# Kernel optimization log

Measured on AMD Instinct MI355X. Metric: run time of the kernel, lower is better.

## Reference

```python
import jax, jax.numpy as jnp
import numpy as np

DT = 0.1
B_SZ = 8192
T_HIST = 20
LEN_PRED = 30
FEAT = 32
N_LAYERS = 3
# state transition for constant-acceleration model (matches self.F in torch)
F_MAT = np.array([[1.0, DT, DT * DT / 2], [0.0, 1.0, DT], [0.0, 0.0, 1.0]], dtype=np.float32)


def setup_inputs() -> dict:
    key = jax.random.key(0)
    ks = jax.random.split(key, 16)
    # random-walk trajectories as history observations
    hist = jnp.cumsum(jax.random.normal(ks[0], (B_SZ, T_HIST, 2), jnp.float32) * 0.5, axis=1)
    k_lin = 1.0 / np.sqrt(FEAT)
    k_in = 1.0 / np.sqrt(24)

    def u(k, shape, scale):
        return jax.random.uniform(k, shape, jnp.float32, -scale, scale)

    return {
        "hist": hist,
        "max_accel_x": jnp.ones((1,), jnp.float32) * 10.0,
        "max_accel_y": jnp.ones((1,), jnp.float32) * 20.0,
        "velocity_std_x": jnp.ones((1,), jnp.float32) * 10.0,
        "acceleration_std_x": jnp.ones((1,), jnp.float32) * 10.0,
        "R_x_": jnp.array([0.0448], jnp.float32),
        "R_y_": jnp.array([0.001], jnp.float32),
        "G_x": jnp.array([0.0059, 0.2981, 0.0393], jnp.float32),
        "G_y": jnp.array([0.0059, 0.2981, 0.0393], jnp.float32) / 5.0,
        "Win_W": u(ks[1], (FEAT, 24), k_in),
        "Win_b": u(ks[2], (FEAT,), k_in),
        "enc_Wih": u(ks[3], (N_LAYERS, 4 * FEAT, FEAT), k_lin),
        "enc_Whh": u(ks[4], (N_LAYERS, 4 * FEAT, FEAT), k_lin),
        "enc_bih": u(ks[5], (N_LAYERS, 4 * FEAT), k_lin),
        "enc_bhh": u(ks[6], (N_LAYERS, 4 * FEAT), k_lin),
        "dec_Wih": u(ks[7], (N_LAYERS, 4 * FEAT, FEAT), k_lin),
        "dec_Whh": u(ks[8], (N_LAYERS, 4 * FEAT, FEAT), k_lin),
        "dec_bih": u(ks[9], (N_LAYERS, 4 * FEAT), k_lin),
        "dec_bhh": u(ks[10], (N_LAYERS, 4 * FEAT), k_lin),
        "Wout_W": u(ks[11], (4, FEAT), k_lin),
        "Wout_b": u(ks[12], (4,), k_lin),
        "len_pred": LEN_PRED,
    }


def reference(hist, max_accel_x, max_accel_y, velocity_std_x, acceleration_std_x,
              R_x_, R_y_, G_x, G_y, Win_W, Win_b,
              enc_Wih, enc_Whh, enc_bih, enc_bhh,
              dec_Wih, dec_Whh, dec_bih, dec_bhh,
              Wout_W, Wout_b, len_pred):
    B = hist.shape[0]
    F = jnp.asarray(F_MAT)
    R_x = R_x_[0] * R_x_[0]
    R_y = R_y_[0] * R_y_[0]
    Z_x = hist[:, :, 0]
    Z_y = hist[:, :, 1]

    def lstm(x, h, c, Wih, Whh, bih, bhh):
        g = x @ Wih.T + bih + h @ Whh.T + bhh
        i, f, gg, o = jnp.split(g, 4, axis=1)
        c = jax.nn.sigmoid(f) * c + jax.nn.sigmoid(i) * jnp.tanh(gg)
        h = jax.nn.sigmoid(o) * jnp.tanh(c)
        return h, c

    def stack(XP, h, c, Wih, Whh, bih, bhh):
        x = jnp.tanh(XP @ Win_W.T + Win_b)
        hs, cs = [], []
        for j in range(N_LAYERS):
            hj, cj = lstm(x, h[j], c[j], Wih[j], Whh[j], bih[j], bhh[j])
            hs.append(hj)
            cs.append(cj)
            x = cj  # torch code feeds the fresh CELL state to the next layer
        return jnp.stack(hs), jnp.stack(cs)

    def kpred(X, P, Q):
        return X @ F.T, jnp.einsum('ij,bjk,lk->bil', F, P, F) + Q

    def kupdate(X, P, z, R):
        y = z - X[:, 0]                      # innovation (H picks component 0)
        S = P[:, 0, 0] + R                   # innovation covariance (scalar)
        K = P[:, :, 0] / S[:, None]          # Kalman gain (B,3)
        return X + y[:, None] * K, P - K[:, :, None] * P[:, 0:1, :]

    def kinit(z0):
        # torch always calls _kalman_init with is_x=True (default), so both
        # axes use R_x / velocity_std_x / acceleration_std_x
        X = jnp.zeros((B, 3), hist.dtype).at[:, 0].set(z0)
        d = jnp.stack([R_x, velocity_std_x[0] ** 2, acceleration_std_x[0] ** 2])
        P = jnp.zeros((B, 3, 3), hist.dtype).at[:, jnp.arange(3), jnp.arange(3)].set(d)
        return X, P

    Qx_e = jnp.outer(G_x * max_accel_x[0], G_x * max_accel_x[0])
    Qy_e = jnp.outer(G_y * max_accel_y[0], G_y * max_accel_y[0])

    Xx, Px = kinit(Z_x[:, 0])
    Xy, Py = kinit(Z_y[:, 0])
    h = jnp.zeros((N_LAYERS, B, FEAT), hist.dtype)
    c = jnp.zeros_like(h)

    def enc_step(carry, zs):
        Xx, Px, Xy, Py, h, c = carry
        zx, zy = zs
        XP = jnp.concatenate([Xx, Xy, Px.reshape(B, 9), Py.reshape(B, 9)], 1)
        h, c = stack(XP, h, c, enc_Wih, enc_Whh, enc_bih, enc_bhh)
        Xx, Px = kpred(Xx, Px, Qx_e)
        Xy, Py = kpred(Xy, Py, Qy_e)
        Xx, Px = kupdate(Xx, Px, zx, R_x)
        Xy, Py = kupdate(Xy, Py, zy, R_y)
        return (Xx, Px, Xy, Py, h, c), None

    carry, _ = jax.lax.scan(enc_step, (Xx, Px, Xy, Py, h, c),
                            (Z_x[:, 1:].T, Z_y[:, 1:].T))

    oxx = jnp.outer(G_x, G_x)
    oyy = jnp.outer(G_y, G_y)

    def dec_step(carry, _):
        Xx, Px, Xy, Py, h, c = carry
        XP = jnp.concatenate([Xx, Xy, Px.reshape(B, 9), Py.reshape(B, 9)], 1)
        h, c = stack(XP, h, c, dec_Wih, dec_Whh, dec_bih, dec_bhh)
        pred = c[-1] @ Wout_W.T + Wout_b  # (B,4): [u_x, u_y, std_x, std_y]
        Xx = Xx.at[:, 2].set(DT * pred[:, 0])  # X[:,2] = B*u
        Xy = Xy.at[:, 2].set(DT * pred[:, 1])
        Qx = (pred[:, 2] ** 2)[:, None, None] * oxx
        Qy = (pred[:, 3] ** 2)[:, None, None] * oyy
        Xx, Px = kpred(Xx, Px, Qx)
        Xy, Py = kpred(Xy, Py, Qy)
        out = jnp.stack([Xx[:, 0], Xy[:, 0],
                         jnp.sqrt(Px[:, 0, 0]), jnp.sqrt(Py[:, 0, 0]),
                         jnp.zeros(B, hist.dtype)], axis=1)  # (B,5)
        return (Xx, Px, Xy, Py, h, c), out

    carry, ys = jax.lax.scan(dec_step, carry, None, length=len_pred)
    return jnp.transpose(ys, (1, 0, 2))  # (B, len_pred, 5)
```

## Files before the change

kernel.cpp:

```cpp
#include <hip/hip_runtime.h>
#include <math.h>

#define DT   0.1f
#define HDT  0.005f
#define T_HIST 20
#define LEN_PRED 30

typedef __attribute__((ext_vector_type(8))) short bfrag8;
typedef __attribute__((ext_vector_type(4))) float f32x4;
typedef __attribute__((ext_vector_type(2))) unsigned int u32x2;

#define WS_FRAG   0u
#define WS_WIN    98304u
#define WS_WOUT   100352u
#define WS_BIAS   101376u

static __device__ __forceinline__ unsigned short f2bf(float x) {
    union { float f; unsigned int u; } v; v.f = x;
    unsigned int r = v.u + 0x7fffu + ((v.u >> 16) & 1u);
    return (unsigned short)(r >> 16);
}

static __device__ __forceinline__ unsigned int cvtpk(float lo, float hi) {
    unsigned int r;
    asm("v_cvt_pk_bf16_f32 %0, %1, %2" : "=v"(r) : "v"(lo), "v"(hi));
    return r;
}

__global__ void prep_kernel(const float* __restrict__ Win_W,
                            const float* __restrict__ eWih, const float* __restrict__ eWhh,
                            const float* __restrict__ ebih, const float* __restrict__ ebhh,
                            const float* __restrict__ dWih, const float* __restrict__ dWhh,
                            const float* __restrict__ dbih, const float* __restrict__ dbhh,
                            const float* __restrict__ Wout_W,
                            char* __restrict__ ws)
{
    int i = blockIdx.x * blockDim.x + threadIdx.x;
    if (i < 49152) {
        int fi = i >> 9, within = i & 511;
        int lane = within >> 3, jj = within & 7;
        int t = fi & 7, c = (fi >> 3) & 1;
        int pl = fi >> 4;
        int l = pl % 3, ph = pl / 3;
        int p = lane & 15, q2 = lane >> 4;
        int gate = p & 3;
        int feat = (t >> 1) * 8 + 2 * (p >> 2) + (t & 1);
        int row = gate * 32 + feat;
        int k = q2 * 8 + jj;
        const float* W = (c == 0) ? (ph ? dWih : eWih) : (ph ? dWhh : eWhh);
        ((unsigned short*)(ws + WS_FRAG))[i] = f2bf(W[l * 4096 + row * 32 + k]);
    } else if (i < 50176) {
        int i2 = i - 49152;
        int w = i2 >> 9, within = i2 & 511;
        int lane = within >> 3, jj = within & 7;
        int p = lane & 15, q2 = lane >> 4;
        int k = q2 * 8 + jj;
        float v = (k < 24) ? Win_W[(w * 16 + p) * 24 + k] : 0.f;
        ((unsigned short*)(ws + WS_WIN))[i2] = f2bf(v);
    } else if (i < 50688) {
        int i3 = i - 50176;
        int lane = i3 >> 3, jj = i3 & 7;
        int p = lane & 15, q2 = lane >> 4;
        float v = Wout_W[(p & 3) * 32 + q2 * 8 + jj];
        ((unsigned short*)(ws + WS_WOUT))[i3] = f2bf(v);
    } else if (i < 51456) {
        int b = i - 50688;
        int ph = b / 384, rem = b % 384;
        int l = rem >> 7, w2 = rem & 127;
        int col = w2 >> 2, r = w2 & 3;
        const float* bi = ph ? dbih : ebih;
        const float* bh = ph ? dbhh : ebhh;
        ((float*)(ws + WS_BIAS))[b] = bi[l * 128 + r * 32 + col] + bh[l * 128 + r * 32 + col];
    }
}

__launch_bounds__(256, 2)
__global__ void kalman_lstm_kernel(const float* __restrict__ hist,
                                   const float* __restrict__ max_ax, const float* __restrict__ max_ay,
                                   const float* __restrict__ vstd, const float* __restrict__ astd,
                                   const float* __restrict__ Rx_, const float* __restrict__ Ry_,
                                   const float* __restrict__ Gx, const float* __restrict__ Gy,
                                   const float* __restrict__ Win_b, const float* __restrict__ Wout_b,
                                   const char* __restrict__ ws, float* __restrict__ out)
{
    __shared__ __align__(16) unsigned int xchC[3][2][4][16][4];
    __shared__ __align__(16) unsigned int xchH[3][2][4][16][4];
    __shared__ __align__(16) unsigned int xenc[T_HIST - 1][4][16][4];
    __shared__ __align__(16) unsigned int x0b[4][16][4];
    __shared__ __align__(16) unsigned int xps[2][4][16][4];

    const int tid  = threadIdx.x;
    const int wv   = tid >> 6;
    const int lane = tid & 63;
    const int q    = lane >> 4;
    const int m    = lane & 15;
    const int be   = blockIdx.x * 16 + m;
    const f32x4 zero4 = {0.f, 0.f, 0.f, 0.f};

    const bfrag8* fragp = (const bfrag8*)(ws + WS_FRAG);
    const f32x4*  biasp = (const f32x4*)(ws + WS_BIAS);

    bfrag8 fragA[3][2][2];
    f32x4  biasV[3][2];
    auto load_phase = [&](int ph) {
#pragma unroll
        for (int l = 0; l < 3; ++l) {
#pragma unroll
            for (int c = 0; c < 2; ++c)
#pragma unroll
                for (int j = 0; j < 2; ++j)
                    fragA[l][c][j] = fragp[(((ph * 3 + l) * 2 + c) * 8 + (2 * wv + j)) * 64 + lane];
#pragma unroll
            for (int j = 0; j < 2; ++j)
                biasV[l][j] = biasp[ph * 96 + l * 32 + (wv * 8 + 2 * q + j)];
        }
    };
    load_phase(0);

    const int w  = (wv >= 2) ? (wv - 2) : 0;
    const int ch = q & 1;
    bfrag8 winF = ((const bfrag8*)(ws + WS_WIN))[w * 64 + lane];
    f32x4 winBv;
#pragma unroll
    for (int r = 0; r < 4; ++r) winBv[r] = Win_b[w * 16 + q * 4 + r];
    bfrag8 woutF = ((const bfrag8*)(ws + WS_WOUT))[lane];
    const float wb0 = Wout_b[0], wb1 = Wout_b[1], wb2 = Wout_b[2], wb3 = Wout_b[3];

    float Rch = 0.f;
    float g00 = 0.f, g01 = 0.f, g02 = 0.f, g11 = 0.f, g12 = 0.f, g22 = 0.f;
    float e00 = 0.f, e01 = 0.f, e02 = 0.f, e11 = 0.f, e12 = 0.f, e22 = 0.f;
    float X0 = 0.f, X1 = 0.f, X2 = 0.f;
    float P00 = 0.f, P01 = 0.f, P02 = 0.f, P11 = 0.f, P12 = 0.f, P22 = 0.f;
    if (wv >= 2) {
        const float rx = Rx_[0] * Rx_[0], ry = Ry_[0] * Ry_[0];
        Rch = ch ? ry : rx;
        float G0, G1, G2, sc;
        if (ch == 0) { G0 = Gx[0]; G1 = Gx[1]; G2 = Gx[2]; sc = max_ax[0]; }
        else         { G0 = Gy[0]; G1 = Gy[1]; G2 = Gy[2]; sc = max_ay[0]; }
        g00 = G0 * G0; g01 = G0 * G1; g02 = G0 * G2;
        g11 = G1 * G1; g12 = G1 * G2; g22 = G2 * G2;
        float s2 = sc * sc;
        e00 = g00 * s2; e01 = g01 * s2; e02 = g02 * s2;
        e11 = g11 * s2; e12 = g12 * s2; e22 = g22 * s2;
        X0 = hist[be * 40 + ch];
        P00 = rx; P11 = vstd[0] * vstd[0]; P22 = astd[0] * astd[0];
    }

    float creg[3][2];
#pragma unroll
    for (int l = 0; l < 3; ++l) { creg[l][0] = 0.f; creg[l][1] = 0.f; }

    auto sig = [](float z) { return __builtin_amdgcn_rcpf(1.f + __expf(-z)); };
    auto th  = [](float z) { return fmaf(-2.f, __builtin_amdgcn_rcpf(__expf(2.f * z) + 1.f), 1.f); };

    auto kpredL = [&](float Q00, float Q01, float Q02, float Q11, float Q12, float Q22) {
        X0 = X0 + DT * X1 + HDT * X2;
        X1 = X1 + DT * X2;
        float M00 = P00 + DT * P01 + HDT * P02;
        float M01 = P01 + DT * P11 + HDT * P12;
        float M02 = P02 + DT * P12 + HDT * P22;
        float M11 = P11 + DT * P12;
        float M12 = P12 + DT * P22;
        float M22 = P22;
        P00 = M00 + DT * M01 + HDT * M02 + Q00;
        P01 = M01 + DT * M02 + Q01;
        P02 = M02 + Q02;
        P11 = M11 + DT * M12 + Q11;
        P12 = M12 + Q12;
        P22 = M22 + Q22;
    };
    auto kupdL = [&](float z) {
        float y = z - X0;
        float Sinv = 1.0f / (P00 + Rch);
        float K0 = P00 * Sinv, K1 = P01 * Sinv, K2 = P02 * Sinv;
        X0 += y * K0; X1 += y * K1; X2 += y * K2;
        float p00 = P00, p01 = P01, p02 = P02;
        P00 = p00 - K0 * p00;
        P01 = p01 - K0 * p01;
        P02 = p02 - K0 * p02;
        P11 = P11 - K1 * p01;
        P12 = P12 - K1 * p02;
        P22 = P22 - K2 * p02;
    };
    auto kf_enc_step = [&](int s) {
        float z = hist[be * 40 + s * 2 + ch];
        kpredL(e00, e01, e02, e11, e12, e22);
        kupdL(z);
    };
    auto stage_xp = [&]() {
        if (q < 2) {
            unsigned short* b = (unsigned short*)&xps[w][0][0][0];
            auto wr = [&](int f, float v) { b[(f >> 3) * 128 + m * 8 + (f & 7)] = f2bf(v); };
            int o = ch * 3;
            wr(o + 0, X0); wr(o + 1, X1); wr(o + 2, X2);
            int pb = 6 + ch * 9;
            wr(pb + 0, P00); wr(pb + 1, P01); wr(pb + 2, P02);
            wr(pb + 3, P01); wr(pb + 4, P11); wr(pb + 5, P12);
            wr(pb + 6, P02); wr(pb + 7, P12); wr(pb + 8, P22);
        }
    };

    auto gates_from = [&](int l, int j, f32x4 a, float& cv, float& hv) {
        float iv = sig(a[0]), fv = sig(a[1]), gv = th(a[2]), ov = sig(a[3]);
        float c = fmaf(fv, creg[l][j], iv * gv);
        creg[l][j] = c;
        cv = c;
        hv = ov * th(c);
    };

    for (int i = tid; i < 3 * 2 * 4 * 16 * 4; i += 256) {
        (&xchC[0][0][0][0][0])[i] = 0;
        (&xchH[0][0][0][0][0])[i] = 0;
    }

    if (wv >= 2) {
        for (int i = lane; i < 4 * 16 * 4; i += 64) (&xps[w][0][0][0])[i] = 0;
#pragma unroll 1
        for (int s = 0; s < T_HIST - 1; ++s) {
            if (s > 0) kf_enc_step(s);
            stage_xp();
            bfrag8 bxp = *(const bfrag8*)&xps[w][q][m][0];
            f32x4 aw = __builtin_amdgcn_mfma_f32_16x16x32_bf16(winF, bxp, winBv, 0, 0, 0);
            float v0 = th(aw[0]), v1 = th(aw[1]), v2 = th(aw[2]), v3 = th(aw[3]);
            u32x2 pk; pk.x = cvtpk(v0, v1); pk.y = cvtpk(v2, v3);
            *(u32x2*)&xenc[s][2 * w + (q >> 1)][m][(q & 1) * 2] = pk;
        }
        kf_enc_step(T_HIST - 1);
    }
    __syncthreads();

#pragma unroll 1
    for (int p = 0; p < T_HIST + 1; ++p) {
        const int pw = p & 1, pr = pw ^ 1;
        const bool b0 = (p <= T_HIST - 2);
        const bool b1 = (p >= 1) && (p <= T_HIST - 1);
        const bool b2 = (p >= 2);
        unsigned int cd0, hd0, cd1, hd1, cd2, hd2;
        if (b0) {
            bfrag8 xf = *(const bfrag8*)&xenc[p][q][m][0];
            bfrag8 hf = *(const bfrag8*)&xchH[0][pr][q][m][0];
            f32x4 a = __builtin_amdgcn_mfma_f32_16x16x32_bf16(fragA[0][1][0], hf, biasV[0][0], 0, 0, 0);
            a = __builtin_amdgcn_mfma_f32_16x16x32_bf16(fragA[0][0][0], xf, a, 0, 0, 0);
            f32x4 b = __builtin_amdgcn_mfma_f32_16x16x32_bf16(fragA[0][1][1], hf, biasV[0][1], 0, 0, 0);
            b = __builtin_amdgcn_mfma_f32_16x16x32_bf16(fragA[0][0][1], xf, b, 0, 0, 0);
            float c0, h0, c1, h1;
            gates_from(0, 0, a, c0, h0); gates_from(0, 1, b, c1, h1);
            cd0 = cvtpk(c0, c1); hd0 = cvtpk(h0, h1);
        }
        if (b1) {
            bfrag8 xf = *(const bfrag8*)&xchC[0][pr][q][m][0];
            bfrag8 hf = *(const bfrag8*)&xchH[1][pr][q][m][0];
            f32x4 a = __builtin_amdgcn_mfma_f32_16x16x32_bf16(fragA[1][1][0], hf, biasV[1][0], 0, 0, 0);
            a = __builtin_amdgcn_mfma_f32_16x16x32_bf16(fragA[1][0][0], xf, a, 0, 0, 0);
            f32x4 b = __builtin_amdgcn_mfma_f32_16x16x32_bf16(fragA[1][1][1], hf, biasV[1][1], 0, 0, 0);
            b = __builtin_amdgcn_mfma_f32_16x16x32_bf16(fragA[1][0][1], xf, b, 0, 0, 0);
            float c0, h0, c1, h1;
            gates_from(1, 0, a, c0, h0); gates_from(1, 1, b, c1, h1);
            cd1 = cvtpk(c0, c1); hd1 = cvtpk(h0, h1);
        }
        if (b2) {
            bfrag8 xf = *(const bfrag8*)&xchC[1][pr][q][m][0];
            bfrag8 hf = *(const bfrag8*)&xchH[2][pr][q][m][0];
            f32x4 a = __builtin_amdgcn_mfma_f32_16x16x32_bf16(fragA[2][1][0], hf, biasV[2][0], 0, 0, 0);
            a = __builtin_amdgcn_mfma_f32_16x16x32_bf16(fragA[2][0][0], xf, a, 0, 0, 0);
            f32x4 b = __builtin_amdgcn_mfma_f32_16x16x32_bf16(fragA[2][1][1], hf, biasV[2][1], 0, 0, 0);
            b = __builtin_amdgcn_mfma_f32_16x16x32_bf16(fragA[2][0][1], xf, b, 0, 0, 0);
            float c0, h0, c1, h1;
            gates_from(2, 0, a, c0, h0); gates_from(2, 1, b, c1, h1);
            cd2 = cvtpk(c0, c1); hd2 = cvtpk(h0, h1);
        }
        if (b0) { xchC[0][pw][wv][m][q] = cd0; xchH[0][pw][wv][m][q] = hd0; }
        if (b1) { xchC[1][pw][wv][m][q] = cd1; xchH[1][pw][wv][m][q] = hd1; }
        if (b2) { xchC[2][pw][wv][m][q] = cd2; xchH[2][pw][wv][m][q] = hd2; }
        __syncthreads();
    }

    load_phase(1);
    bfrag8 hfragR[3];
    hfragR[0] = *(const bfrag8*)&xchH[0][0][q][m][0];
    hfragR[1] = *(const bfrag8*)&xchH[1][1][q][m][0];
    hfragR[2] = *(const bfrag8*)&xchH[2][0][q][m][0];
    bfrag8 c2f = *(const bfrag8*)&xchC[2][0][q][m][0];

    auto do_pred = [&](int tout) {
        f32x4 ap = __builtin_amdgcn_mfma_f32_16x16x32_bf16(woutF, c2f, zero4, 0, 0, 0);
        float pe = ch ? (ap[1] + wb1) : (ap[0] + wb0);
        float qe = ch ? (ap[3] + wb3) : (ap[2] + wb2);
        X2 = DT * pe;
        float qs = qe * qe;
        kpredL(qs * g00, qs * g01, qs * g02, qs * g11, qs * g12, qs * g22);
        if (wv == 2 && q < 2) {
            float* o = out + (size_t)be * (LEN_PRED * 5) + tout * 5;
            if (ch == 0) { o[0] = X0; o[2] = sqrtf(P00); }
            else         { o[1] = X0; o[3] = sqrtf(P00); o[4] = 0.f; }
        }
    };

#pragma unroll 1
    for (int t = 0; t < LEN_PRED; ++t) {
        f32x4 ah[3][2];
#pragma unroll
        for (int l = 0; l < 3; ++l)
#pragma unroll
            for (int j = 0; j < 2; ++j)
                ah[l][j] = __builtin_amdgcn_mfma_f32_16x16x32_bf16(fragA[l][1][j], hfragR[l], biasV[l][j], 0, 0, 0);

        if (wv >= 2) {
            if (t > 0) do_pred(t - 1);
            stage_xp();
            bfrag8 bxp = *(const bfrag8*)&xps[w][q][m][0];
            f32x4 aw = __builtin_amdgcn_mfma_f32_16x16x32_bf16(winF, bxp, winBv, 0, 0, 0);
            float v0 = th(aw[0]), v1 = th(aw[1]), v2 = th(aw[2]), v3 = th(aw[3]);
            u32x2 pk; pk.x = cvtpk(v0, v1); pk.y = cvtpk(v2, v3);
            *(u32x2*)&x0b[2 * w + (q >> 1)][m][(q & 1) * 2] = pk;
        }
        __syncthreads();

        bfrag8 xf = *(const bfrag8*)&x0b[q][m][0];
#pragma unroll
        for (int l = 0; l < 3; ++l) {
            f32x4 a0 = __builtin_amdgcn_mfma_f32_16x16x32_bf16(fragA[l][0][0], xf, ah[l][0], 0, 0, 0);
            f32x4 a1 = __builtin_amdgcn_mfma_f32_16x16x32_bf16(fragA[l][0][1], xf, ah[l][1], 0, 0, 0);
            float c0, h0, c1, h1;
            gates_from(l, 0, a0, c0, h0);
            gates_from(l, 1, a1, c1, h1);
            xchC[l][0][wv][m][q] = cvtpk(c0, c1);
            xchH[l][0][wv][m][q] = cvtpk(h0, h1);
            __syncthreads();
            xf        = *(const bfrag8*)&xchC[l][0][q][m][0];
            hfragR[l] = *(const bfrag8*)&xchH[l][0][q][m][0];
        }
        c2f = xf;
    }
    do_pred(LEN_PRED - 1);
}

extern "C" void kernel_launch(void* const* d_in, const int* in_sizes, int n_in,
                              void* d_out, int out_size, void* d_ws, size_t ws_size,
                              hipStream_t stream)
{
    const float* hist  = (const float*)d_in[0];
    const float* maxax = (const float*)d_in[1];
    const float* maxay = (const float*)d_in[2];
    const float* vstd  = (const float*)d_in[3];
    const float* astd  = (const float*)d_in[4];
    const float* Rx    = (const float*)d_in[5];
    const float* Ry    = (const float*)d_in[6];
    const float* Gx    = (const float*)d_in[7];
    const float* Gy    = (const float*)d_in[8];
    const float* WinW  = (const float*)d_in[9];
    const float* Winb  = (const float*)d_in[10];
    const float* eWih  = (const float*)d_in[11];
    const float* eWhh  = (const float*)d_in[12];
    const float* ebih  = (const float*)d_in[13];
    const float* ebhh  = (const float*)d_in[14];
    const float* dWih  = (const float*)d_in[15];
    const float* dWhh  = (const float*)d_in[16];
    const float* dbih  = (const float*)d_in[17];
    const float* dbhh  = (const float*)d_in[18];
    const float* WoutW = (const float*)d_in[19];
    const float* Woutb = (const float*)d_in[20];
    char* ws = (char*)d_ws;
    float* out = (float*)d_out;

    prep_kernel<<<202, 256, 0, stream>>>(WinW, eWih, eWhh, ebih, ebhh,
                                         dWih, dWhh, dbih, dbhh, WoutW, ws);
    kalman_lstm_kernel<<<512, 256, 0, stream>>>(hist, maxax, maxay, vstd, astd,
                                                Rx, Ry, Gx, Gy, Winb, Woutb,
                                                ws, out);
}
```

Before: 184.7 us.

## Fold Kalman predict into input projection to remove per-step LDS staging and barrier

```diff
diff --git a/kernel.cpp b/kernel.cpp
--- a/kernel.cpp
+++ b/kernel.cpp
@@ -80,14 +80,13 @@
                                    const float* __restrict__ vstd, const float* __restrict__ astd,
                                    const float* __restrict__ Rx_, const float* __restrict__ Ry_,
                                    const float* __restrict__ Gx, const float* __restrict__ Gy,
-                                   const float* __restrict__ Win_b, const float* __restrict__ Wout_b,
+                                   const float* __restrict__ Win_W, const float* __restrict__ Win_b,
+                                   const float* __restrict__ Wout_b,
                                    const char* __restrict__ ws, float* __restrict__ out)
 {
     __shared__ __align__(16) unsigned int xchC[3][2][4][16][4];
     __shared__ __align__(16) unsigned int xchH[3][2][4][16][4];
     __shared__ __align__(16) unsigned int xenc[T_HIST - 1][4][16][4];
-    __shared__ __align__(16) unsigned int x0b[4][16][4];
-    __shared__ __align__(16) unsigned int xps[2][4][16][4];
 
     const int tid  = threadIdx.x;
     const int wv   = tid >> 6;
@@ -117,8 +116,7 @@
     };
     load_phase(0);
 
-    const int w  = (wv >= 2) ? (wv - 2) : 0;
-    const int ch = q & 1;
+    const int w = (wv >= 2) ? (wv - 2) : 0;
     bfrag8 winF = ((const bfrag8*)(ws + WS_WIN))[w * 64 + lane];
     f32x4 winBv;
 #pragma unroll
@@ -126,24 +124,92 @@
     bfrag8 woutF = ((const bfrag8*)(ws + WS_WOUT))[lane];
     const float wb0 = Wout_b[0], wb1 = Wout_b[1], wb2 = Wout_b[2], wb3 = Wout_b[3];
 
-    float Rch = 0.f;
-    float g00 = 0.f, g01 = 0.f, g02 = 0.f, g11 = 0.f, g12 = 0.f, g22 = 0.f;
-    float e00 = 0.f, e01 = 0.f, e02 = 0.f, e11 = 0.f, e12 = 0.f, e22 = 0.f;
-    float X0 = 0.f, X1 = 0.f, X2 = 0.f;
-    float P00 = 0.f, P01 = 0.f, P02 = 0.f, P11 = 0.f, P12 = 0.f, P22 = 0.f;
-    if (wv >= 2) {
-        const float rx = Rx_[0] * Rx_[0], ry = Ry_[0] * Ry_[0];
-        Rch = ch ? ry : rx;
-        float G0, G1, G2, sc;
-        if (ch == 0) { G0 = Gx[0]; G1 = Gx[1]; G2 = Gx[2]; sc = max_ax[0]; }
-        else         { G0 = Gy[0]; G1 = Gy[1]; G2 = Gy[2]; sc = max_ay[0]; }
-        g00 = G0 * G0; g01 = G0 * G1; g02 = G0 * G2;
-        g11 = G1 * G1; g12 = G1 * G2; g22 = G2 * G2;
-        float s2 = sc * sc;
-        e00 = g00 * s2; e01 = g01 * s2; e02 = g02 * s2;
-        e11 = g11 * s2; e12 = g12 * s2; e22 = g22 * s2;
-        X0 = hist[be * 40 + ch];
-        P00 = rx; P11 = vstd[0] * vstd[0]; P22 = astd[0] * astd[0];
+    const float rx = Rx_[0] * Rx_[0], ry = Ry_[0] * Ry_[0];
+    const float gX0 = Gx[0], gX1 = Gx[1], gX2 = Gx[2];
+    const float gY0 = Gy[0], gY1 = Gy[1], gY2 = Gy[2];
+    const float gx00 = gX0*gX0, gx01 = gX0*gX1, gx02 = gX0*gX2,
+                gx11 = gX1*gX1, gx12 = gX1*gX2, gx22 = gX2*gX2;
+    const float gy00 = gY0*gY0, gy01 = gY0*gY1, gy02 = gY0*gY2,
+                gy11 = gY1*gY1, gy12 = gY1*gY2, gy22 = gY2*gY2;
+    const float sx2 = max_ax[0] * max_ax[0], sy2 = max_ay[0] * max_ay[0];
+    const float ex00 = gx00*sx2, ex01 = gx01*sx2, ex02 = gx02*sx2,
+                ex11 = gx11*sx2, ex12 = gx12*sx2, ex22 = gx22*sx2;
+    const float ey00 = gy00*sy2, ey01 = gy01*sy2, ey02 = gy02*sy2,
+                ey11 = gy11*sy2, ey12 = gy12*sy2, ey22 = gy22*sy2;
+    const float pv = vstd[0] * vstd[0], pa = astd[0] * astd[0];
+
+    float Xx0 = hist[be * 40 + 0], Xx1 = 0.f, Xx2 = 0.f;
+    float Xy0 = hist[be * 40 + 1], Xy1 = 0.f, Xy2 = 0.f;
+    float Px00 = rx, Px01 = 0.f, Px02 = 0.f, Px11 = pv, Px12 = 0.f, Px22 = pa;
+    float Py00 = rx, Py01 = 0.f, Py02 = 0.f, Py11 = pv, Py12 = 0.f, Py22 = pa;
+
+    bfrag8 winAf[2], winPf[2];
+    f32x4  winCb[2];
+    float wpx[8], wpy[8], wqx[8], wqy[8];
+    {
+        auto applyA_col = [&](int k, float* col) {
+            float in[24];
+#pragma unroll
+            for (int j = 0; j < 24; ++j) in[j] = (j == k) ? 1.f : 0.f;
+            col[0] = in[0] + DT * in[1]; col[1] = in[1]; col[2] = 0.f;
+            col[3] = in[3] + DT * in[4]; col[4] = in[4]; col[5] = 0.f;
+#pragma unroll
+            for (int b = 0; b < 2; ++b) {
+                int o = 6 + b * 9;
+                float M[3][3];
+#pragma unroll
+                for (int j = 0; j < 3; ++j) {
+                    M[0][j] = in[o + j] + DT * in[o + 3 + j] + HDT * in[o + 6 + j];
+                    M[1][j] = in[o + 3 + j] + DT * in[o + 6 + j];
+                    M[2][j] = in[o + 6 + j];
+                }
+#pragma unroll
+                for (int i = 0; i < 3; ++i) {
+                    col[o + 3 * i + 0] = M[i][0] + DT * M[i][1] + HDT * M[i][2];
+                    col[o + 3 * i + 1] = M[i][1] + DT * M[i][2];
+                    col[o + 3 * i + 2] = M[i][2];
+                }
+            }
+        };
+        union { bfrag8 f; unsigned short s[8]; } ua, up;
+#pragma unroll
+        for (int t = 0; t < 2; ++t) {
+            int feat = 8 * (m >> 2) + 4 * t + (m & 3);
+            const float* wr = Win_W + feat * 24;
+#pragma unroll
+            for (int jj = 0; jj < 8; ++jj) {
+                int k = q * 8 + jj;
+                float va = 0.f, vp = 0.f;
+                if (k < 24) {
+                    float col[24];
+                    applyA_col(k, col);
+                    vp = wr[k];
+#pragma unroll
+                    for (int j = 0; j < 24; ++j) va += wr[j] * col[j];
+                }
+                ua.s[jj] = f2bf(va);
+                up.s[jj] = f2bf(vp);
+            }
+            winAf[t] = ua.f;
+            winPf[t] = up.f;
+#pragma unroll
+            for (int r = 0; r < 4; ++r) winCb[t][r] = Win_b[8 * q + 4 * t + r];
+        }
+#pragma unroll
+        for (int e = 0; e < 8; ++e) {
+            const float* wr = Win_W + (8 * q + e) * 24;
+            wpx[e] = wr[0] * (HDT * DT) + wr[1] * (DT * DT) + wr[2] * DT;
+            wpy[e] = wr[3] * (HDT * DT) + wr[4] * (DT * DT) + wr[5] * DT;
+            float sx = 0.f, sy = 0.f;
+#pragma unroll
+            for (int i2 = 0; i2 < 3; ++i2)
+#pragma unroll
+                for (int j2 = 0; j2 < 3; ++j2) {
+                    sx += wr[6 + 3 * i2 + j2]  * (Gx[i2] * Gx[j2]);
+                    sy += wr[15 + 3 * i2 + j2] * (Gy[i2] * Gy[j2]);
+                }
+            wqx[e] = sx; wqy[e] = sy;
+        }
     }
 
     float creg[3][2];
@@ -153,7 +219,9 @@
     auto sig = [](float z) { return __builtin_amdgcn_rcpf(1.f + __expf(-z)); };
     auto th  = [](float z) { return fmaf(-2.f, __builtin_amdgcn_rcpf(__expf(2.f * z) + 1.f), 1.f); };
 
-    auto kpredL = [&](float Q00, float Q01, float Q02, float Q11, float Q12, float Q22) {
+    auto kpred9 = [](float& X0, float& X1, float& X2,
+                     float& P00, float& P01, float& P02, float& P11, float& P12, float& P22,
+                     float Q00, float Q01, float Q02, float Q11, float Q12, float Q22) {
         X0 = X0 + DT * X1 + HDT * X2;
         X1 = X1 + DT * X2;
         float M00 = P00 + DT * P01 + HDT * P02;
@@ -169,9 +237,11 @@
         P12 = M12 + Q12;
         P22 = M22 + Q22;
     };
-    auto kupdL = [&](float z) {
+    auto kupd9 = [](float& X0, float& X1, float& X2,
+                    float& P00, float& P01, float& P02, float& P11, float& P12, float& P22,
+                    float z, float R) {
         float y = z - X0;
-        float Sinv = 1.0f / (P00 + Rch);
+        float Sinv = 1.0f / (P00 + R);
         float K0 = P00 * Sinv, K1 = P01 * Sinv, K2 = P02 * Sinv;
         X0 += y * K0; X1 += y * K1; X2 += y * K2;
         float p00 = P00, p01 = P01, p02 = P02;
@@ -183,21 +253,26 @@
         P22 = P22 - K2 * p02;
     };
     auto kf_enc_step = [&](int s) {
-        float z = hist[be * 40 + s * 2 + ch];
-        kpredL(e00, e01, e02, e11, e12, e22);
-        kupdL(z);
-    };
-    auto stage_xp = [&]() {
-        if (q < 2) {
-            unsigned short* b = (unsigned short*)&xps[w][0][0][0];
-            auto wr = [&](int f, float v) { b[(f >> 3) * 128 + m * 8 + (f & 7)] = f2bf(v); };
-            int o = ch * 3;
-            wr(o + 0, X0); wr(o + 1, X1); wr(o + 2, X2);
-            int pb = 6 + ch * 9;
-            wr(pb + 0, P00); wr(pb + 1, P01); wr(pb + 2, P02);
-            wr(pb + 3, P01); wr(pb + 4, P11); wr(pb + 5, P12);
-            wr(pb + 6, P02); wr(pb + 7, P12); wr(pb + 8, P22);
-        }
+        float zx = hist[be * 40 + s * 2], zy = hist[be * 40 + s * 2 + 1];
+        kpred9(Xx0, Xx1, Xx2, Px00, Px01, Px02, Px11, Px12, Px22, ex00, ex01, ex02, ex11, ex12, ex22);
+        kupd9 (Xx0, Xx1, Xx2, Px00, Px01, Px02, Px11, Px12, Px22, zx, rx);
+        kpred9(Xy0, Xy1, Xy2, Py00, Py01, Py02, Py11, Py12, Py22, ey00, ey01, ey02, ey11, ey12, ey22);
+        kupd9 (Xy0, Xy1, Xy2, Py00, Py01, Py02, Py11, Py12, Py22, zy, ry);
+    };
+
+    auto packf = [&](const float* v) {
+        union { bfrag8 f; unsigned int u[4]; } u;
+#pragma unroll
+        for (int d = 0; d < 4; ++d) u.u[d] = cvtpk(v[2 * d], v[2 * d + 1]);
+        return u.f;
+    };
+    auto build_xp = [&]() {
+        float v[8];
+        if (q == 0)      { v[0]=Xx0;  v[1]=Xx1;  v[2]=Xx2;  v[3]=Xy0;  v[4]=Xy1;  v[5]=Xy2;  v[6]=Px00; v[7]=Px01; }
+        else if (q == 1) { v[0]=Px02; v[1]=Px01; v[2]=Px11; v[3]=Px12; v[4]=Px02; v[5]=Px12; v[6]=Px22; v[7]=Py00; }
+        else if (q == 2) { v[0]=Py01; v[1]=Py02; v[2]=Py01; v[3]=Py11; v[4]=Py12; v[5]=Py02; v[6]=Py12; v[7]=Py22; }
+        else             { v[0]=0.f; v[1]=0.f; v[2]=0.f; v[3]=0.f; v[4]=0.f; v[5]=0.f; v[6]=0.f; v[7]=0.f; }
+        return packf(v);
     };
 
     auto gates_from = [&](int l, int j, f32x4 a, float& cv, float& hv) {
@@ -213,20 +288,17 @@
         (&xchH[0][0][0][0][0])[i] = 0;
     }
 
-    if (wv >= 2) {
-        for (int i = lane; i < 4 * 16 * 4; i += 64) (&xps[w][0][0][0])[i] = 0;
 #pragma unroll 1
-        for (int s = 0; s < T_HIST - 1; ++s) {
-            if (s > 0) kf_enc_step(s);
-            stage_xp();
-            bfrag8 bxp = *(const bfrag8*)&xps[w][q][m][0];
-            f32x4 aw = __builtin_amdgcn_mfma_f32_16x16x32_bf16(winF, bxp, winBv, 0, 0, 0);
-            float v0 = th(aw[0]), v1 = th(aw[1]), v2 = th(aw[2]), v3 = th(aw[3]);
-            u32x2 pk; pk.x = cvtpk(v0, v1); pk.y = cvtpk(v2, v3);
+    for (int s = 0; s < T_HIST - 1; ++s) {
+        if (s > 0) kf_enc_step(s);
+        if (wv >= 2) {
+            bfrag8 xpf = build_xp();
+            f32x4 aw = __builtin_amdgcn_mfma_f32_16x16x32_bf16(winF, xpf, winBv, 0, 0, 0);
+            u32x2 pk; pk.x = cvtpk(th(aw[0]), th(aw[1])); pk.y = cvtpk(th(aw[2]), th(aw[3]));
             *(u32x2*)&xenc[s][2 * w + (q >> 1)][m][(q & 1) * 2] = pk;
         }
-        kf_enc_step(T_HIST - 1);
-    }
+    }
+    kf_enc_step(T_HIST - 1);
     __syncthreads();
 
 #pragma unroll 1
@@ -282,41 +354,47 @@
     hfragR[2] = *(const bfrag8*)&xchH[2][0][q][m][0];
     bfrag8 c2f = *(const bfrag8*)&xchC[2][0][q][m][0];
 
-    auto do_pred = [&](int tout) {
-        f32x4 ap = __builtin_amdgcn_mfma_f32_16x16x32_bf16(woutF, c2f, zero4, 0, 0, 0);
-        float pe = ch ? (ap[1] + wb1) : (ap[0] + wb0);
-        float qe = ch ? (ap[3] + wb3) : (ap[2] + wb2);
-        X2 = DT * pe;
-        float qs = qe * qe;
-        kpredL(qs * g00, qs * g01, qs * g02, qs * g11, qs * g12, qs * g22);
-        if (wv == 2 && q < 2) {
-            float* o = out + (size_t)be * (LEN_PRED * 5) + tout * 5;
-            if (ch == 0) { o[0] = X0; o[2] = sqrtf(P00); }
-            else         { o[1] = X0; o[3] = sqrtf(P00); o[4] = 0.f; }
-        }
-    };
-
+    bfrag8 xp = build_xp();
+    f32x4 wp0 = __builtin_amdgcn_mfma_f32_16x16x32_bf16(winPf[0], xp, winCb[0], 0, 0, 0);
+    f32x4 wp1 = __builtin_amdgcn_mfma_f32_16x16x32_bf16(winPf[1], xp, winCb[1], 0, 0, 0);
+    __syncthreads();
+
+    float px = 0.f, py = 0.f, qsx = 0.f, qsy = 0.f;
 #pragma unroll 1
     for (int t = 0; t < LEN_PRED; ++t) {
+        if (t > 0) {
+            f32x4 ap = __builtin_amdgcn_mfma_f32_16x16x32_bf16(woutF, c2f, zero4, 0, 0, 0);
+            px = ap[0] + wb0; py = ap[1] + wb1;
+            float qe2 = ap[2] + wb2, qe3 = ap[3] + wb3;
+            qsx = qe2 * qe2; qsy = qe3 * qe3;
+        }
+        float xv[8];
+#pragma unroll
+        for (int e = 0; e < 8; ++e) {
+            float pre = (e < 4) ? wp0[e] : wp1[e - 4];
+            xv[e] = th(fmaf(px, wpx[e], fmaf(py, wpy[e], fmaf(qsx, wqx[e], fmaf(qsy, wqy[e], pre)))));
+        }
+        bfrag8 xf = packf(xv);
         f32x4 ah[3][2];
 #pragma unroll
         for (int l = 0; l < 3; ++l)
 #pragma unroll
             for (int j = 0; j < 2; ++j)
                 ah[l][j] = __builtin_amdgcn_mfma_f32_16x16x32_bf16(fragA[l][1][j], hfragR[l], biasV[l][j], 0, 0, 0);
-
-        if (wv >= 2) {
-            if (t > 0) do_pred(t - 1);
-            stage_xp();
-            bfrag8 bxp = *(const bfrag8*)&xps[w][q][m][0];
-            f32x4 aw = __builtin_amdgcn_mfma_f32_16x16x32_bf16(winF, bxp, winBv, 0, 0, 0);
-            float v0 = th(aw[0]), v1 = th(aw[1]), v2 = th(aw[2]), v3 = th(aw[3]);
-            u32x2 pk; pk.x = cvtpk(v0, v1); pk.y = cvtpk(v2, v3);
-            *(u32x2*)&x0b[2 * w + (q >> 1)][m][(q & 1) * 2] = pk;
-        }
-        __syncthreads();
-
-        bfrag8 xf = *(const bfrag8*)&x0b[q][m][0];
+        if (t > 0) {
+            Xx2 = DT * px; Xy2 = DT * py;
+            kpred9(Xx0, Xx1, Xx2, Px00, Px01, Px02, Px11, Px12, Px22,
+                   qsx*gx00, qsx*gx01, qsx*gx02, qsx*gx11, qsx*gx12, qsx*gx22);
+            kpred9(Xy0, Xy1, Xy2, Py00, Py01, Py02, Py11, Py12, Py22,
+                   qsy*gy00, qsy*gy01, qsy*gy02, qsy*gy11, qsy*gy12, qsy*gy22);
+            if (wv == 0 && q == 0) {
+                float* o = out + (size_t)be * (LEN_PRED * 5) + (t - 1) * 5;
+                o[0] = Xx0; o[1] = Xy0; o[2] = sqrtf(Px00); o[3] = sqrtf(Py00); o[4] = 0.f;
+            }
+        }
+        xp = build_xp();
+        wp0 = __builtin_amdgcn_mfma_f32_16x16x32_bf16(winAf[0], xp, winCb[0], 0, 0, 0);
+        wp1 = __builtin_amdgcn_mfma_f32_16x16x32_bf16(winAf[1], xp, winCb[1], 0, 0, 0);
 #pragma unroll
         for (int l = 0; l < 3; ++l) {
             f32x4 a0 = __builtin_amdgcn_mfma_f32_16x16x32_bf16(fragA[l][0][0], xf, ah[l][0], 0, 0, 0);
@@ -332,7 +410,21 @@
         }
         c2f = xf;
     }
-    do_pred(LEN_PRED - 1);
+    {
+        f32x4 ap = __builtin_amdgcn_mfma_f32_16x16x32_bf16(woutF, c2f, zero4, 0, 0, 0);
+        px = ap[0] + wb0; py = ap[1] + wb1;
+        float qe2 = ap[2] + wb2, qe3 = ap[3] + wb3;
+        qsx = qe2 * qe2; qsy = qe3 * qe3;
+        Xx2 = DT * px; Xy2 = DT * py;
+        kpred9(Xx0, Xx1, Xx2, Px00, Px01, Px02, Px11, Px12, Px22,
+               qsx*gx00, qsx*gx01, qsx*gx02, qsx*gx11, qsx*gx12, qsx*gx22);
+        kpred9(Xy0, Xy1, Xy2, Py00, Py01, Py02, Py11, Py12, Py22,
+               qsy*gy00, qsy*gy01, qsy*gy02, qsy*gy11, qsy*gy12, qsy*gy22);
+        if (wv == 0 && q == 0) {
+            float* o = out + (size_t)be * (LEN_PRED * 5) + (LEN_PRED - 1) * 5;
+            o[0] = Xx0; o[1] = Xy0; o[2] = sqrtf(Px00); o[3] = sqrtf(Py00); o[4] = 0.f;
+        }
+    }
 }
 
 extern "C" void kernel_launch(void* const* d_in, const int* in_sizes, int n_in,
@@ -366,6 +458,6 @@
     prep_kernel<<<202, 256, 0, stream>>>(WinW, eWih, eWhh, ebih, ebhh,
                                          dWih, dWhh, dbih, dbhh, WoutW, ws);
     kalman_lstm_kernel<<<512, 256, 0, stream>>>(hist, maxax, maxay, vstd, astd,
-                                                Rx, Ry, Gx, Gy, Winb, Woutb,
+                                                Rx, Ry, Gx, Gy, WinW, Winb, Woutb,
                                                 ws, out);
 }
```

Result: slower. 218.4 us (+18.2%).
